# Kernel optimization log

Measured on AMD Instinct MI355X. Metric: run time of the kernel, lower is better.

Reference implementation:

```python
import jax, jax.numpy as jnp
import numpy as np

EPROJS = 512
ODIM = 1024
DLAYERS = 2
DUNITS = 512
EMBED_DIM = 512
JOINT_DIM = 512
BLANK = 0
B, TMAX, LMAX = 4, 256, 63


def setup_inputs() -> dict:
    key = jax.random.key(0)
    ks = jax.random.split(key, 20)
    s = 0.05
    embed = jax.random.normal(ks[0], (ODIM, EMBED_DIM), jnp.float32) * s
    embed = embed.at[BLANK].set(0.0)  # padding_idx=blank
    inp = {
        "hs_pad": jax.random.normal(ks[1], (B, TMAX, EPROJS), jnp.float32),
        "hlens": jnp.full((B,), TMAX, jnp.int32),
        "ys_pad": jax.random.randint(ks[2], (B, LMAX), 0, ODIM, jnp.int64),
        "embed": embed,
        "W_ih0": jax.random.normal(ks[3], (4 * DUNITS, EMBED_DIM), jnp.float32) * s,
        "W_hh0": jax.random.normal(ks[4], (4 * DUNITS, DUNITS), jnp.float32) * s,
        "b_ih0": jax.random.normal(ks[5], (4 * DUNITS,), jnp.float32) * s,
        "b_hh0": jax.random.normal(ks[6], (4 * DUNITS,), jnp.float32) * s,
        "W_ih1": jax.random.normal(ks[7], (4 * DUNITS, DUNITS), jnp.float32) * s,
        "W_hh1": jax.random.normal(ks[8], (4 * DUNITS, DUNITS), jnp.float32) * s,
        "b_ih1": jax.random.normal(ks[9], (4 * DUNITS,), jnp.float32) * s,
        "b_hh1": jax.random.normal(ks[10], (4 * DUNITS,), jnp.float32) * s,
        "W_enc": jax.random.normal(ks[11], (JOINT_DIM, EPROJS), jnp.float32) * s,
        "b_enc": jax.random.normal(ks[12], (JOINT_DIM,), jnp.float32) * s,
        "W_dec": jax.random.normal(ks[13], (JOINT_DIM, DUNITS), jnp.float32) * s,
        "W_out": jax.random.normal(ks[14], (ODIM, JOINT_DIM), jnp.float32) * s,
        "b_out": jax.random.normal(ks[15], (ODIM,), jnp.float32) * s,
    }
    return inp


def _lstm_cell(x, h, c, Wih, Whh, bih, bhh):
    g = x @ Wih.T + bih + h @ Whh.T + bhh  # (B, 4*dunits)
    i, f, gg, o = jnp.split(g, 4, axis=-1)  # torch gate order: i, f, g, o
    c2 = jax.nn.sigmoid(f) * c + jax.nn.sigmoid(i) * jnp.tanh(gg)
    h2 = jax.nn.sigmoid(o) * jnp.tanh(c2)
    return h2, c2


def reference(hs_pad, hlens, ys_pad, embed, W_ih0, W_hh0, b_ih0, b_hh0,
              W_ih1, W_hh1, b_ih1, b_hh1, W_enc, b_enc, W_dec, W_out, b_out):
    Bsz = hs_pad.shape[0]
    # ys_in = [blank] + ys  (dropout is eval-mode identity)
    blank_col = jnp.full((Bsz, 1), BLANK, ys_pad.dtype)
    ys_in = jnp.concatenate([blank_col, ys_pad], axis=1)  # (B, U)
    eys = embed[ys_in]  # (B, U, E)

    def step(carry, ey):
        h0, c0, h1, c1 = carry
        h0, c0 = _lstm_cell(ey, h0, c0, W_ih0, W_hh0, b_ih0, b_hh0)
        h1, c1 = _lstm_cell(h0, h1, c1, W_ih1, W_hh1, b_ih1, b_hh1)
        return (h0, c0, h1, c1), h1

    z0 = jnp.zeros((Bsz, DUNITS), hs_pad.dtype)
    _, h_dec = jax.lax.scan(step, (z0, z0, z0, z0), jnp.swapaxes(eys, 0, 1))
    h_dec = jnp.swapaxes(h_dec, 0, 1)  # (B, U, dunits)

    # joint: tanh(lin_enc(h_enc) + lin_dec(h_dec)) -> lin_out
    henc = hs_pad @ W_enc.T + b_enc          # (B, T, J)
    hdec = h_dec @ W_dec.T                   # (B, U, J)
    z = jnp.tanh(henc[:, :, None, :] + hdec[:, None, :, :])  # (B, T, U, J)
    return z @ W_out.T + b_out               # (B, T, U, odim)
```

## Files before the change

### kernel.cpp

```cpp
#include <hip/hip_runtime.h>
#include <hip/hip_bf16.h>
#include <cstdint>
#include <cstddef>

#define DEVINL __device__ __forceinline__

typedef _Float16 f16x8 __attribute__((ext_vector_type(8)));
typedef _Float16 f16x2 __attribute__((ext_vector_type(2)));
typedef float    f32x4 __attribute__((ext_vector_type(4)));

#define SENT 0xFFFFFFFFFFFFFFFFull


DEVINL float fsigm(float x) {
    float e = __expf(-x);
    return __builtin_amdgcn_rcpf(1.f + e);
}
DEVINL float ftanh(float x) {
    float e = __expf(2.f * x);
    return 1.f - 2.f * __builtin_amdgcn_rcpf(e + 1.f);
}

DEVINL float dot8(f16x8 w, f16x8 x, float acc) {
    f16x2 w0{w[0], w[1]}, w1{w[2], w[3]}, w2{w[4], w[5]}, w3{w[6], w[7]};
    f16x2 x0{x[0], x[1]}, x1{x[2], x[3]}, x2{x[4], x[5]}, x3{x[6], x[7]};
    acc = __builtin_amdgcn_fdot2(w0, x0, acc, false);
    acc = __builtin_amdgcn_fdot2(w1, x1, acc, false);
    acc = __builtin_amdgcn_fdot2(w2, x2, acc, false);
    acc = __builtin_amdgcn_fdot2(w3, x3, acc, false);
    return acc;
}

DEVINL void pollrows(const _Float16* __restrict__ H, int slot, int kp,
                     f16x8 out[4][2]) {
    const uint64_t* base = (const uint64_t*)H + (size_t)slot * 512;
    uint64_t w[16];
    for (;;) {
        bool bad = false;
        #pragma unroll
        for (int b = 0; b < 4; ++b) {
            const uint64_t* rp = base + b * 128 + kp * 2;
            w[b * 4 + 0] = __hip_atomic_load(rp,      __ATOMIC_RELAXED, __HIP_MEMORY_SCOPE_AGENT);
            w[b * 4 + 1] = __hip_atomic_load(rp + 1,  __ATOMIC_RELAXED, __HIP_MEMORY_SCOPE_AGENT);
            w[b * 4 + 2] = __hip_atomic_load(rp + 64, __ATOMIC_RELAXED, __HIP_MEMORY_SCOPE_AGENT);
            w[b * 4 + 3] = __hip_atomic_load(rp + 65, __ATOMIC_RELAXED, __HIP_MEMORY_SCOPE_AGENT);
        }
        #pragma unroll
        for (int i = 0; i < 16; ++i) bad |= (w[i] == SENT);
        if (!bad) break;
        __builtin_amdgcn_s_sleep(1);
    }
    #pragma unroll
    for (int b = 0; b < 4; ++b) {
        union { uint64_t u[2]; f16x8 v; } u0, u1;
        u0.u[0] = w[b * 4 + 0]; u0.u[1] = w[b * 4 + 1];
        u1.u[0] = w[b * 4 + 2]; u1.u[1] = w[b * 4 + 3];
        out[b][0] = u0.v;
        out[b][1] = u1.v;
    }
}

__global__ void k_prep_f16(const float* __restrict__ wih0, const float* __restrict__ whh0,
                           const float* __restrict__ wih1, const float* __restrict__ whh1,
                           const float* __restrict__ wout, _Float16* __restrict__ dst, int total) {
    int stride = gridDim.x * blockDim.x;
    for (int i = blockIdx.x * blockDim.x + threadIdx.x; i < total; i += stride) {
        const float* src; int off;
        if      (i < (1 << 20)) { src = wih0; off = i; }
        else if (i < (2 << 20)) { src = whh0; off = i - (1 << 20); }
        else if (i < (3 << 20)) { src = wih1; off = i - (2 << 20); }
        else if (i < (4 << 20)) { src = whh1; off = i - (3 << 20); }
        else                    { src = wout; off = i - (4 << 20); }
        dst[i] = (_Float16)src[off];
    }
}

__global__ void k_embed(const float* __restrict__ embed, const int* __restrict__ ys,
                        _Float16* __restrict__ Ebuf) {
    int bu = blockIdx.x;
    int b = bu >> 6, u = bu & 63;
    int tok = (u == 0) ? 0 : ys[b * 63 + (u - 1)];
    const float* src = embed + (size_t)tok * 512;
    _Float16* dst = Ebuf + ((size_t)(u * 4 + b)) * 512;
    int t2 = threadIdx.x * 2;
    float2 v = *(const float2*)(src + t2);
    dst[t2]     = (_Float16)v.x;
    dst[t2 + 1] = (_Float16)v.y;
}

__global__ void __launch_bounds__(256, 1) k_lstm(
        const _Float16* __restrict__ WF,
        const float* __restrict__ bih0, const float* __restrict__ bhh0,
        const float* __restrict__ bih1, const float* __restrict__ bhh1,
        const _Float16* __restrict__ Ebuf,
        _Float16* __restrict__ H0h, _Float16* __restrict__ H1h,
        float* __restrict__ H1) {
    const int blk   = blockIdx.x;
    const int layer = blk >> 5;
    const int ublk  = blk & 31;
    const int unit0 = ublk * 16;
    const int tid   = threadIdx.x;
    const int rg    = tid >> 5;
    const int kp    = tid & 31;

    const int rb_own   = rg * 8 + (kp >> 2);
    const int b_own    = kp & 3;
    const int grow_own = ((rb_own >> 4) << 9) + unit0 + (rb_own & 15);

    const _Float16* WihL = WF + (size_t)(layer ? (2u << 20) : 0u);
    const _Float16* WhhL = WF + (size_t)(layer ? (3u << 20) : (1u << 20));

    f16x8 wA[8][2];
    f16x8 wB[8][2];
    #pragma unroll
    for (int r = 0; r < 8; ++r) {
        int rb = rg * 8 + r;
        int grow = ((rb >> 4) << 9) + unit0 + (rb & 15);
        const _Float16* irow = WihL + (size_t)grow * 512;
        const _Float16* hrow = WhhL + (size_t)grow * 512;
        wA[r][0] = *(const f16x8*)(irow + kp * 8);
        wA[r][1] = *(const f16x8*)(irow + 256 + kp * 8);
        wB[r][0] = *(const f16x8*)(hrow + kp * 8);
        wB[r][1] = *(const f16x8*)(hrow + 256 + kp * 8);
    }
    const float* biL = layer ? bih1 : bih0;
    const float* bhL = layer ? bhh1 : bhh0;
    const float bsum = biL[grow_own] + bhL[grow_own];

    __shared__ float g_lds[64 * 4];

    float c_reg = 0.f;
    const int c0 = kp * 8;
    const int c1 = 256 + kp * 8;
    const int s_lo = layer ? 1 : 0;
    const int s_hi = layer ? 64 : 63;

    for (int s = s_lo; s <= s_hi; ++s) {
        const int st = s - s_lo;

        float p[8][4];
        #pragma unroll
        for (int r = 0; r < 8; ++r)
            #pragma unroll
            for (int b = 0; b < 4; ++b) p[r][b] = 0.f;

        if (!layer) {
            #pragma unroll
            for (int b = 0; b < 4; ++b) {
                const _Float16* er = Ebuf + ((size_t)(st * 4 + b)) * 512;
                f16x8 x0 = *(const f16x8*)(er + c0);
                f16x8 x1 = *(const f16x8*)(er + c1);
                #pragma unroll
                for (int r = 0; r < 8; ++r) {
                    p[r][b] = dot8(wA[r][0], x0, p[r][b]);
                    p[r][b] = dot8(wA[r][1], x1, p[r][b]);
                }
            }
            if (st > 0) {
                f16x8 hv[4][2];
                pollrows(H0h, st - 1, kp, hv);
                #pragma unroll
                for (int b = 0; b < 4; ++b)
                    #pragma unroll
                    for (int r = 0; r < 8; ++r) {
                        p[r][b] = dot8(wB[r][0], hv[b][0], p[r][b]);
                        p[r][b] = dot8(wB[r][1], hv[b][1], p[r][b]);
                    }
            }
        } else {
            f16x8 xv[4][2];
            pollrows(H0h, st, kp, xv);
            #pragma unroll
            for (int b = 0; b < 4; ++b)
                #pragma unroll
                for (int r = 0; r < 8; ++r) {
                    p[r][b] = dot8(wA[r][0], xv[b][0], p[r][b]);
                    p[r][b] = dot8(wA[r][1], xv[b][1], p[r][b]);
                }
            if (st > 0) {
                f16x8 hv[4][2];
                pollrows(H1h, st - 1, kp, hv);
                #pragma unroll
                for (int b = 0; b < 4; ++b)
                    #pragma unroll
                    for (int r = 0; r < 8; ++r) {
                        p[r][b] = dot8(wB[r][0], hv[b][0], p[r][b]);
                        p[r][b] = dot8(wB[r][1], hv[b][1], p[r][b]);
                    }
            }
        }

        float a[32];
        #pragma unroll
        for (int t = 0; t < 32; ++t) a[t] = p[t >> 2][t & 3];
        #pragma unroll
        for (int m = 16; m >= 1; m >>= 1) {
            const bool hi = (kp & m) != 0;
            #pragma unroll
            for (int i = 0; i < m; ++i) {
                float give = hi ? a[i] : a[i + m];
                float got  = __shfl_xor(give, m, 64);
                a[i] = (hi ? a[i + m] : a[i]) + got;
            }
        }
        g_lds[rb_own * 4 + b_own] = a[0] + bsum;
        __syncthreads();

        if (tid < 64) {
            int jj = tid >> 2, b4 = tid & 3;
            float gi = g_lds[(0  + jj) * 4 + b4];
            float gf = g_lds[(16 + jj) * 4 + b4];
            float gg = g_lds[(32 + jj) * 4 + b4];
            float go = g_lds[(48 + jj) * 4 + b4];
            c_reg = fsigm(gf) * c_reg + fsigm(gi) * ftanh(gg);
            float h2 = fsigm(go) * ftanh(c_reg);
            _Float16 h16 = (_Float16)h2;
            unsigned short hb;
            __builtin_memcpy(&hb, &h16, 2);
            int hv0 = (int)hb;
            int hv1 = __shfl_down(hv0, 4, 64);
            int hv2 = __shfl_down(hv0, 8, 64);
            int hv3 = __shfl_down(hv0, 12, 64);
            if ((jj & 3) == 0) {
                uint64_t pk = (uint64_t)(hv0 & 0xFFFF)
                            | ((uint64_t)(hv1 & 0xFFFF) << 16)
                            | ((uint64_t)(hv2 & 0xFFFF) << 32)
                            | ((uint64_t)(hv3 & 0xFFFF) << 48);
                _Float16* dst = (layer ? H1h : H0h) + (size_t)((st << 2) + b4) * 512 + unit0 + jj;
                __hip_atomic_store((uint64_t*)dst, pk,
                                   __ATOMIC_RELAXED, __HIP_MEMORY_SCOPE_AGENT);
            }
            if (layer) {
                int hu = unit0 + jj;
                __hip_atomic_store(H1 + ((size_t)(b4 * 64 + st)) * 512 + hu, h2,
                                   __ATOMIC_RELAXED, __HIP_MEMORY_SCOPE_AGENT);
            }
        }
        __syncthreads();
    }
}

__global__ void __launch_bounds__(256) k_gemm_small(
        const float* __restrict__ A, const float* __restrict__ Bt,
        const float* __restrict__ bias, float* __restrict__ C) {
    __shared__ float As[64 * 68];
    __shared__ float Bs[64 * 68];
    int bn = blockIdx.x & 7;
    int bm = blockIdx.x >> 3;
    int m0 = bm * 64, n0 = bn * 64;
    int tid = threadIdx.x;
    int tx = tid & 15, ty = tid >> 4;
    float acc[4][4] = {};
    for (int k0 = 0; k0 < 512; k0 += 64) {
        __syncthreads();
        #pragma unroll
        for (int i = 0; i < 4; ++i) {
            int fid = i * 256 + tid;
            int rr = fid >> 4, c4 = (fid & 15) * 4;
            *(float4*)(As + rr * 68 + c4) = *(const float4*)(A + (size_t)(m0 + rr) * 512 + k0 + c4);
            *(float4*)(Bs + rr * 68 + c4) = *(const float4*)(Bt + (size_t)(n0 + rr) * 512 + k0 + c4);
        }
        __syncthreads();
        #pragma unroll 4
        for (int kk = 0; kk < 64; kk += 4) {
            float4 a4[4], b4[4];
            #pragma unroll
            for (int ii = 0; ii < 4; ++ii) a4[ii] = *(const float4*)(As + (ty + ii * 16) * 68 + kk);
            #pragma unroll
            for (int jjx = 0; jjx < 4; ++jjx) b4[jjx] = *(const float4*)(Bs + (tx + jjx * 16) * 68 + kk);
            #pragma unroll
            for (int ii = 0; ii < 4; ++ii)
                #pragma unroll
                for (int jjx = 0; jjx < 4; ++jjx)
                    acc[ii][jjx] += a4[ii].x * b4[jjx].x + a4[ii].y * b4[jjx].y +
                                    a4[ii].z * b4[jjx].z + a4[ii].w * b4[jjx].w;
        }
    }
    #pragma unroll
    for (int ii = 0; ii < 4; ++ii) {
        int m = m0 + ty + ii * 16;
        #pragma unroll
        for (int jjx = 0; jjx < 4; ++jjx) {
            int n = n0 + tx + jjx * 16;
            float v = acc[ii][jjx] + (bias ? bias[n] : 0.f);
            C[(size_t)m * 512 + n] = v;
        }
    }
}

__global__ void __launch_bounds__(256) k_joint(
        const float* __restrict__ henc, const float* __restrict__ hdec,
        const _Float16* __restrict__ Wo, const float* __restrict__ b_out,
        float* __restrict__ out) {
    __shared__ _Float16 As[128 * 72];
    __shared__ _Float16 Bs[128 * 72];

    const int bn = blockIdx.x & 7;
    const int bm = blockIdx.x >> 3;
    const int m0 = bm * 128, n0 = bn * 128;
    const int b  = m0 >> 14;
    const int t0 = (m0 & 16383) >> 6;

    const int tid  = threadIdx.x;
    const int wave = tid >> 6, lane = tid & 63;
    const int wm = wave >> 1, wn = wave & 1;
    const int l16 = lane & 15, quad = lane >> 4;

    const int r_gen = tid >> 1;
    const int half  = tid & 1;
    const int tg = r_gen >> 6, ug = r_gen & 63;
    const float* he_row = henc + ((size_t)(b * 256 + t0 + tg)) * 512 + half * 32;
    const float* hd_row = hdec + ((size_t)(b * 64 + ug)) * 512 + half * 32;
    _Float16* As_row = As + r_gen * 72 + half * 32;

    f32x4 acc[4][4];
    #pragma unroll
    for (int i = 0; i < 4; ++i)
        #pragma unroll
        for (int jx = 0; jx < 4; ++jx) acc[i][jx] = f32x4{0.f, 0.f, 0.f, 0.f};

    for (int kit = 0; kit < 8; ++kit) {
        const int k0 = kit * 64;
        __syncthreads();
        #pragma unroll
        for (int i2 = 0; i2 < 4; ++i2) {
            float4 a  = *(const float4*)(he_row + k0 + i2 * 8);
            float4 c  = *(const float4*)(hd_row + k0 + i2 * 8);
            float4 a2 = *(const float4*)(he_row + k0 + i2 * 8 + 4);
            float4 c2 = *(const float4*)(hd_row + k0 + i2 * 8 + 4);
            f16x8 z8;
            z8[0] = (_Float16)ftanh(a.x + c.x);
            z8[1] = (_Float16)ftanh(a.y + c.y);
            z8[2] = (_Float16)ftanh(a.z + c.z);
            z8[3] = (_Float16)ftanh(a.w + c.w);
            z8[4] = (_Float16)ftanh(a2.x + c2.x);
            z8[5] = (_Float16)ftanh(a2.y + c2.y);
            z8[6] = (_Float16)ftanh(a2.z + c2.z);
            z8[7] = (_Float16)ftanh(a2.w + c2.w);
            *(f16x8*)(As_row + i2 * 8) = z8;
        }
        #pragma unroll
        for (int j2 = 0; j2 < 4; ++j2) {
            int q = j2 * 256 + tid;
            int rr = q >> 3, c8 = q & 7;
            f16x8 w = *(const f16x8*)(Wo + (size_t)(n0 + rr) * 512 + k0 + c8 * 8);
            *(f16x8*)(Bs + rr * 72 + c8 * 8) = w;
        }
        __syncthreads();
        #pragma unroll
        for (int kk = 0; kk < 64; kk += 32) {
            f16x8 af[4], bfv[4];
            #pragma unroll
            for (int i = 0; i < 4; ++i)
                af[i] = *(const f16x8*)(As + (wm * 64 + i * 16 + l16) * 72 + kk + quad * 8);
            #pragma unroll
            for (int jx = 0; jx < 4; ++jx)
                bfv[jx] = *(const f16x8*)(Bs + (wn * 64 + jx * 16 + l16) * 72 + kk + quad * 8);
            #pragma unroll
            for (int i = 0; i < 4; ++i)
                #pragma unroll
                for (int jx = 0; jx < 4; ++jx)
                    acc[i][jx] = __builtin_amdgcn_mfma_f32_16x16x32_f16(af[i], bfv[jx], acc[i][jx], 0, 0, 0);
        }
    }
    #pragma unroll
    for (int i = 0; i < 4; ++i) {
        int mrow = m0 + wm * 64 + i * 16 + quad * 4;
        #pragma unroll
        for (int jx = 0; jx < 4; ++jx) {
            int col = n0 + wn * 64 + jx * 16 + l16;
            float bo = b_out[col];
            float* po = out + (size_t)mrow * 1024 + col;
            po[0]    = acc[i][jx][0] + bo;
            po[1024] = acc[i][jx][1] + bo;
            po[2048] = acc[i][jx][2] + bo;
            po[3072] = acc[i][jx][3] + bo;
        }
    }
}

extern "C" void kernel_launch(void* const* d_in, const int* in_sizes, int n_in,
                              void* d_out, int out_size, void* d_ws, size_t ws_size,
                              hipStream_t stream) {
    const float* hs    = (const float*)d_in[0];
    const int*   ys    = (const int*)d_in[2];
    const float* embed = (const float*)d_in[3];
    const float* wih0  = (const float*)d_in[4];
    const float* whh0  = (const float*)d_in[5];
    const float* bih0  = (const float*)d_in[6];
    const float* bhh0  = (const float*)d_in[7];
    const float* wih1  = (const float*)d_in[8];
    const float* whh1  = (const float*)d_in[9];
    const float* bih1  = (const float*)d_in[10];
    const float* bhh1  = (const float*)d_in[11];
    const float* wenc  = (const float*)d_in[12];
    const float* benc  = (const float*)d_in[13];
    const float* wdec  = (const float*)d_in[14];
    const float* wout  = (const float*)d_in[15];
    const float* bout  = (const float*)d_in[16];
    float* out = (float*)d_out;

    char* ws = (char*)d_ws;
    _Float16* WF     = (_Float16*)(ws);
    _Float16* Ebuf16 = (_Float16*)(ws + 9u  * 1024 * 1024);
    _Float16* H0h    = (_Float16*)(ws + 9u  * 1024 * 1024 + 512u * 1024);
    _Float16* H1h    = (_Float16*)(ws + 9u  * 1024 * 1024 + 768u * 1024);
    float* H1    = (float*)(ws + 10u * 1024 * 1024);
    float* henc  = (float*)(ws + 10u * 1024 * 1024 + 512u * 1024);
    float* hdec  = (float*)(ws + 12u * 1024 * 1024 + 512u * 1024);

    hipMemsetAsync(ws + 9u * 1024 * 1024 + 512u * 1024, 0xFF, 512u * 1024, stream);
    k_prep_f16<<<2048, 256, 0, stream>>>(wih0, whh0, wih1, whh1, wout, WF, 4718592);
    k_embed<<<256, 256, 0, stream>>>(embed, ys, Ebuf16);
    k_lstm<<<64, 256, 0, stream>>>(WF, bih0, bhh0, bih1, bhh1, Ebuf16, H0h, H1h, H1);
    k_gemm_small<<<128, 256, 0, stream>>>(hs, wenc, benc, henc);
    k_gemm_small<<<32, 256, 0, stream>>>(H1, wdec, nullptr, hdec);
    k_joint<<<4096, 256, 0, stream>>>(henc, hdec, WF + (4u << 20), bout, out);
}
```

Baseline: 748.3 us.

## Compute joint tanh tile once per block and overlap encoder GEMM with LSTM

The joint kernel now builds the full 128x512 tanh(henc+hdec) A tile in swizzled LDS once per block. It then loops over all 1024 output columns, reading W_out fragments straight from global/L2, where before it recomputed tanh for every 128-column tile and staged W_out through LDS. This removes the 8x redundant tanh and henc/hdec reads but uses 128 KB of LDS per block with one block per CU and no LDS staging for B. Separately, the encoder projection GEMM is folded into the LSTM launch as extra blocks so it runs concurrently with the serial recurrence, though those blocks now carry the LSTM kernel's register budget.

```diff
diff --git a/kernel.cpp b/kernel.cpp
--- a/kernel.cpp
+++ b/kernel.cpp
@@ -88,13 +88,73 @@
     dst[t2 + 1] = (_Float16)v.y;
 }
 
+DEVINL void gemm_small_body(const float* __restrict__ A, const float* __restrict__ Bt,
+                            const float* __restrict__ bias, float* __restrict__ C,
+                            int blk) {
+    __shared__ float As[64 * 68];
+    __shared__ float Bs[64 * 68];
+    int bn = blk & 7;
+    int bm = blk >> 3;
+    int m0 = bm * 64, n0 = bn * 64;
+    int tid = threadIdx.x;
+    int tx = tid & 15, ty = tid >> 4;
+    float acc[4][4] = {};
+    for (int k0 = 0; k0 < 512; k0 += 64) {
+        __syncthreads();
+        #pragma unroll
+        for (int i = 0; i < 4; ++i) {
+            int fid = i * 256 + tid;
+            int rr = fid >> 4, c4 = (fid & 15) * 4;
+            *(float4*)(As + rr * 68 + c4) = *(const float4*)(A + (size_t)(m0 + rr) * 512 + k0 + c4);
+            *(float4*)(Bs + rr * 68 + c4) = *(const float4*)(Bt + (size_t)(n0 + rr) * 512 + k0 + c4);
+        }
+        __syncthreads();
+        #pragma unroll 4
+        for (int kk = 0; kk < 64; kk += 4) {
+            float4 a4[4], b4[4];
+            #pragma unroll
+            for (int ii = 0; ii < 4; ++ii) a4[ii] = *(const float4*)(As + (ty + ii * 16) * 68 + kk);
+            #pragma unroll
+            for (int jjx = 0; jjx < 4; ++jjx) b4[jjx] = *(const float4*)(Bs + (tx + jjx * 16) * 68 + kk);
+            #pragma unroll
+            for (int ii = 0; ii < 4; ++ii)
+                #pragma unroll
+                for (int jjx = 0; jjx < 4; ++jjx)
+                    acc[ii][jjx] += a4[ii].x * b4[jjx].x + a4[ii].y * b4[jjx].y +
+                                    a4[ii].z * b4[jjx].z + a4[ii].w * b4[jjx].w;
+        }
+    }
+    #pragma unroll
+    for (int ii = 0; ii < 4; ++ii) {
+        int m = m0 + ty + ii * 16;
+        #pragma unroll
+        for (int jjx = 0; jjx < 4; ++jjx) {
+            int n = n0 + tx + jjx * 16;
+            float v = acc[ii][jjx] + (bias ? bias[n] : 0.f);
+            C[(size_t)m * 512 + n] = v;
+        }
+    }
+}
+
+__global__ void __launch_bounds__(256) k_gemm_small(
+        const float* __restrict__ A, const float* __restrict__ Bt,
+        const float* __restrict__ bias, float* __restrict__ C) {
+    gemm_small_body(A, Bt, bias, C, blockIdx.x);
+}
+
 __global__ void __launch_bounds__(256, 1) k_lstm(
         const _Float16* __restrict__ WF,
         const float* __restrict__ bih0, const float* __restrict__ bhh0,
         const float* __restrict__ bih1, const float* __restrict__ bhh1,
         const _Float16* __restrict__ Ebuf,
         _Float16* __restrict__ H0h, _Float16* __restrict__ H1h,
-        float* __restrict__ H1) {
+        float* __restrict__ H1,
+        const float* __restrict__ hs, const float* __restrict__ wenc,
+        const float* __restrict__ benc, float* __restrict__ henc) {
+    if (blockIdx.x >= 64) {
+        gemm_small_body(hs, wenc, benc, henc, blockIdx.x - 64);
+        return;
+    }
     const int blk   = blockIdx.x;
     const int layer = blk >> 5;
     const int ublk  = blk & 31;
@@ -240,94 +300,34 @@
     }
 }
 
-__global__ void __launch_bounds__(256) k_gemm_small(
-        const float* __restrict__ A, const float* __restrict__ Bt,
-        const float* __restrict__ bias, float* __restrict__ C) {
-    __shared__ float As[64 * 68];
-    __shared__ float Bs[64 * 68];
-    int bn = blockIdx.x & 7;
-    int bm = blockIdx.x >> 3;
-    int m0 = bm * 64, n0 = bn * 64;
-    int tid = threadIdx.x;
-    int tx = tid & 15, ty = tid >> 4;
-    float acc[4][4] = {};
-    for (int k0 = 0; k0 < 512; k0 += 64) {
-        __syncthreads();
-        #pragma unroll
-        for (int i = 0; i < 4; ++i) {
-            int fid = i * 256 + tid;
-            int rr = fid >> 4, c4 = (fid & 15) * 4;
-            *(float4*)(As + rr * 68 + c4) = *(const float4*)(A + (size_t)(m0 + rr) * 512 + k0 + c4);
-            *(float4*)(Bs + rr * 68 + c4) = *(const float4*)(Bt + (size_t)(n0 + rr) * 512 + k0 + c4);
-        }
-        __syncthreads();
-        #pragma unroll 4
-        for (int kk = 0; kk < 64; kk += 4) {
-            float4 a4[4], b4[4];
-            #pragma unroll
-            for (int ii = 0; ii < 4; ++ii) a4[ii] = *(const float4*)(As + (ty + ii * 16) * 68 + kk);
-            #pragma unroll
-            for (int jjx = 0; jjx < 4; ++jjx) b4[jjx] = *(const float4*)(Bs + (tx + jjx * 16) * 68 + kk);
-            #pragma unroll
-            for (int ii = 0; ii < 4; ++ii)
-                #pragma unroll
-                for (int jjx = 0; jjx < 4; ++jjx)
-                    acc[ii][jjx] += a4[ii].x * b4[jjx].x + a4[ii].y * b4[jjx].y +
-                                    a4[ii].z * b4[jjx].z + a4[ii].w * b4[jjx].w;
-        }
-    }
-    #pragma unroll
-    for (int ii = 0; ii < 4; ++ii) {
-        int m = m0 + ty + ii * 16;
-        #pragma unroll
-        for (int jjx = 0; jjx < 4; ++jjx) {
-            int n = n0 + tx + jjx * 16;
-            float v = acc[ii][jjx] + (bias ? bias[n] : 0.f);
-            C[(size_t)m * 512 + n] = v;
-        }
-    }
-}
-
-__global__ void __launch_bounds__(256) k_joint(
+__global__ void __launch_bounds__(512, 1) k_joint(
         const float* __restrict__ henc, const float* __restrict__ hdec,
         const _Float16* __restrict__ Wo, const float* __restrict__ b_out,
         float* __restrict__ out) {
-    __shared__ _Float16 As[128 * 72];
-    __shared__ _Float16 Bs[128 * 72];
-
-    const int bn = blockIdx.x & 7;
-    const int bm = blockIdx.x >> 3;
-    const int m0 = bm * 128, n0 = bn * 128;
-    const int b  = m0 >> 14;
-    const int t0 = (m0 & 16383) >> 6;
-
-    const int tid  = threadIdx.x;
-    const int wave = tid >> 6, lane = tid & 63;
-    const int wm = wave >> 1, wn = wave & 1;
-    const int l16 = lane & 15, quad = lane >> 4;
-
-    const int r_gen = tid >> 1;
-    const int half  = tid & 1;
-    const int tg = r_gen >> 6, ug = r_gen & 63;
-    const float* he_row = henc + ((size_t)(b * 256 + t0 + tg)) * 512 + half * 32;
-    const float* hd_row = hdec + ((size_t)(b * 64 + ug)) * 512 + half * 32;
-    _Float16* As_row = As + r_gen * 72 + half * 32;
-
-    f32x4 acc[4][4];
-    #pragma unroll
-    for (int i = 0; i < 4; ++i)
-        #pragma unroll
-        for (int jx = 0; jx < 4; ++jx) acc[i][jx] = f32x4{0.f, 0.f, 0.f, 0.f};
-
-    for (int kit = 0; kit < 8; ++kit) {
-        const int k0 = kit * 64;
-        __syncthreads();
-        #pragma unroll
-        for (int i2 = 0; i2 < 4; ++i2) {
-            float4 a  = *(const float4*)(he_row + k0 + i2 * 8);
-            float4 c  = *(const float4*)(hd_row + k0 + i2 * 8);
-            float4 a2 = *(const float4*)(he_row + k0 + i2 * 8 + 4);
-            float4 c2 = *(const float4*)(hd_row + k0 + i2 * 8 + 4);
+    __shared__ _Float16 As[128 * 512];
+
+    const int d   = blockIdx.x;
+    const int bm  = (d & 7) * 64 + (d >> 3);
+    const int m0  = bm * 128;
+    const int b   = m0 >> 14;
+    const int t0  = (m0 & 16383) >> 6;
+    const int tid = threadIdx.x;
+
+    {
+        const int r  = tid >> 2;
+        const int kq = tid & 3;
+        const int t  = t0 + (r >> 6);
+        const int u  = r & 63;
+        const float* he = henc + ((size_t)(b * 256 + t)) * 512 + kq * 128;
+        const float* hd = hdec + ((size_t)(b * 64 + u)) * 512 + kq * 128;
+        _Float16* dst = As + r * 512;
+        const int swz = r & 7;
+        #pragma unroll
+        for (int i = 0; i < 16; ++i) {
+            float4 a  = *(const float4*)(he + i * 8);
+            float4 a2 = *(const float4*)(he + i * 8 + 4);
+            float4 c  = *(const float4*)(hd + i * 8);
+            float4 c2 = *(const float4*)(hd + i * 8 + 4);
             f16x8 z8;
             z8[0] = (_Float16)ftanh(a.x + c.x);
             z8[1] = (_Float16)ftanh(a.y + c.y);
@@ -337,44 +337,61 @@
             z8[5] = (_Float16)ftanh(a2.y + c2.y);
             z8[6] = (_Float16)ftanh(a2.z + c2.z);
             z8[7] = (_Float16)ftanh(a2.w + c2.w);
-            *(f16x8*)(As_row + i2 * 8) = z8;
-        }
-        #pragma unroll
-        for (int j2 = 0; j2 < 4; ++j2) {
-            int q = j2 * 256 + tid;
-            int rr = q >> 3, c8 = q & 7;
-            f16x8 w = *(const f16x8*)(Wo + (size_t)(n0 + rr) * 512 + k0 + c8 * 8);
-            *(f16x8*)(Bs + rr * 72 + c8 * 8) = w;
-        }
-        __syncthreads();
-        #pragma unroll
-        for (int kk = 0; kk < 64; kk += 32) {
+            int cs = (kq * 16 + i) ^ swz;
+            *(f16x8*)(dst + cs * 8) = z8;
+        }
+    }
+    __syncthreads();
+
+    const int wave = tid >> 6, lane = tid & 63;
+    const int l16 = lane & 15, quad = lane >> 4;
+    const int wm = wave >> 2;
+    const int wn = wave & 3;
+    const int swr = l16 & 7;
+
+    for (int nc = 0; nc < 4; ++nc) {
+        f32x4 acc[4][4];
+        #pragma unroll
+        for (int i = 0; i < 4; ++i)
+            #pragma unroll
+            for (int jx = 0; jx < 4; ++jx) acc[i][jx] = f32x4{0.f, 0.f, 0.f, 0.f};
+        const int n_base = nc * 256 + wn * 64;
+
+        #pragma unroll 4
+        for (int step = 0; step < 16; ++step) {
+            const int k0 = step * 32;
+            const int cs = (step * 4 + quad) ^ swr;
             f16x8 af[4], bfv[4];
             #pragma unroll
-            for (int i = 0; i < 4; ++i)
-                af[i] = *(const f16x8*)(As + (wm * 64 + i * 16 + l16) * 72 + kk + quad * 8);
-            #pragma unroll
-            for (int jx = 0; jx < 4; ++jx)
-                bfv[jx] = *(const f16x8*)(Bs + (wn * 64 + jx * 16 + l16) * 72 + kk + quad * 8);
+            for (int i = 0; i < 4; ++i) {
+                int row = wm * 64 + i * 16 + l16;
+                af[i] = *(const f16x8*)(As + row * 512 + cs * 8);
+            }
+            #pragma unroll
+            for (int jx = 0; jx < 4; ++jx) {
+                int n = n_base + jx * 16 + l16;
+                bfv[jx] = *(const f16x8*)(Wo + (size_t)n * 512 + k0 + quad * 8);
+            }
             #pragma unroll
             for (int i = 0; i < 4; ++i)
                 #pragma unroll
                 for (int jx = 0; jx < 4; ++jx)
                     acc[i][jx] = __builtin_amdgcn_mfma_f32_16x16x32_f16(af[i], bfv[jx], acc[i][jx], 0, 0, 0);
         }
-    }
-    #pragma unroll
-    for (int i = 0; i < 4; ++i) {
-        int mrow = m0 + wm * 64 + i * 16 + quad * 4;
-        #pragma unroll
-        for (int jx = 0; jx < 4; ++jx) {
-            int col = n0 + wn * 64 + jx * 16 + l16;
-            float bo = b_out[col];
-            float* po = out + (size_t)mrow * 1024 + col;
-            po[0]    = acc[i][jx][0] + bo;
-            po[1024] = acc[i][jx][1] + bo;
-            po[2048] = acc[i][jx][2] + bo;
-            po[3072] = acc[i][jx][3] + bo;
+
+        #pragma unroll
+        for (int i = 0; i < 4; ++i) {
+            int mrow = m0 + wm * 64 + i * 16 + quad * 4;
+            #pragma unroll
+            for (int jx = 0; jx < 4; ++jx) {
+                int col = n_base + jx * 16 + l16;
+                float bo = b_out[col];
+                float* po = out + (size_t)mrow * 1024 + col;
+                po[0]    = acc[i][jx][0] + bo;
+                po[1024] = acc[i][jx][1] + bo;
+                po[2048] = acc[i][jx][2] + bo;
+                po[3072] = acc[i][jx][3] + bo;
+            }
         }
     }
 }
@@ -412,8 +429,8 @@
     hipMemsetAsync(ws + 9u * 1024 * 1024 + 512u * 1024, 0xFF, 512u * 1024, stream);
     k_prep_f16<<<2048, 256, 0, stream>>>(wih0, whh0, wih1, whh1, wout, WF, 4718592);
     k_embed<<<256, 256, 0, stream>>>(embed, ys, Ebuf16);
-    k_lstm<<<64, 256, 0, stream>>>(WF, bih0, bhh0, bih1, bhh1, Ebuf16, H0h, H1h, H1);
-    k_gemm_small<<<128, 256, 0, stream>>>(hs, wenc, benc, henc);
+    k_lstm<<<192, 256, 0, stream>>>(WF, bih0, bhh0, bih1, bhh1, Ebuf16,
+                                    H0h, H1h, H1, hs, wenc, benc, henc);
     k_gemm_small<<<32, 256, 0, stream>>>(H1, wdec, nullptr, hdec);
-    k_joint<<<4096, 256, 0, stream>>>(henc, hdec, WF + (4u << 20), bout, out);
-}
+    k_joint<<<512, 512, 0, stream>>>(henc, hdec, WF + (4u << 20), bout, out);
+}
```

After: 688.8 us. -7.9%, faster.
